# Kernel optimization log

Hardware: AMD Instinct MI355X
Metric: run time of the kernel (lower is better)

## Reference

```python
import jax, jax.numpy as jnp
import numpy as np
import math

B, N, D, H = 32, 512, 512, 8
DK = D // H
MAX_DIST = 100.0
BINS = 20
BIN_SIZE = MAX_DIST / BINS


def setup_inputs() -> dict:
    key = jax.random.key(0)
    ks = jax.random.split(key, 12)
    s = 1.0 / math.sqrt(D)
    inp = {
        "x": jax.random.normal(ks[0], (B, N, D), dtype=jnp.float32),
        "distance_matrix": jax.random.uniform(ks[1], (B, N, N), dtype=jnp.float32) * MAX_DIST,
        "Wq": jax.random.uniform(ks[2], (D, D), jnp.float32, -s, s),
        "bq": jax.random.uniform(ks[3], (D,), jnp.float32, -s, s),
        "Wk": jax.random.uniform(ks[4], (D, D), jnp.float32, -s, s),
        "bk": jax.random.uniform(ks[5], (D,), jnp.float32, -s, s),
        "Wv": jax.random.uniform(ks[6], (D, D), jnp.float32, -s, s),
        "bv": jax.random.uniform(ks[7], (D,), jnp.float32, -s, s),
        "Wo": jax.random.uniform(ks[8], (D, D), jnp.float32, -s, s),
        "bo": jax.random.uniform(ks[9], (D,), jnp.float32, -s, s),
        "dist_weights": jnp.ones((BINS + 1,), dtype=jnp.float32),
    }
    return inp


def reference(x, distance_matrix, Wq, bq, Wk, bk, Wv, bv, Wo, bo, dist_weights):
    temperature = 1.0
    # Linear projections; torch nn.Linear computes x @ W.T + b
    q = (x @ Wq.T + bq).reshape(B, N, H, DK).transpose(0, 2, 1, 3)  # [B,H,N,DK]
    k = (x @ Wk.T + bk).reshape(B, N, H, DK).transpose(0, 2, 1, 3)
    v = (x @ Wv.T + bv).reshape(B, N, H, DK).transpose(0, 2, 1, 3)

    scores = jnp.einsum("bhqd,bhkd->bhqk", q, k) / math.sqrt(DK)  # [B,H,N,N]

    # Relative position bias: bin distances, look up scalar weight per pair
    binned = jnp.clip((distance_matrix / BIN_SIZE).astype(jnp.int32), 0, BINS)  # [B,N,N]
    bias = dist_weights[binned] / temperature  # [B,N,N]
    scores = scores + bias[:, None, :, :]  # broadcast over heads

    attn = jax.nn.softmax(scores, axis=-1)  # dropout is identity in eval
    out = jnp.einsum("bhqk,bhkd->bhqd", attn, v)  # [B,H,N,DK]
    out = out.transpose(0, 2, 1, 3).reshape(B, N, D)
    return out @ Wo.T + bo
```

## Files before the change

kernel.cpp:

```cpp
#include <hip/hip_runtime.h>
#include <hip/hip_fp16.h>
#include <math.h>
#include <stdint.h>

#define BB 32
#define NN 512
#define DDIM 512
#define HH 8
#define DK 64

typedef __attribute__((ext_vector_type(8))) short short8;
typedef __attribute__((ext_vector_type(8))) _Float16 half8;
typedef __attribute__((ext_vector_type(2))) _Float16 half2v;
typedef __attribute__((ext_vector_type(4))) float floatx4;
typedef unsigned short ushort_t;
typedef unsigned int uint_t;

__device__ __forceinline__ void gl_lds16(const void* g, void* l) {
    __builtin_amdgcn_global_load_lds(
        (const __attribute__((address_space(1))) uint_t*)g,
        (__attribute__((address_space(3))) uint_t*)l,
        16, 0, 0);
}

__device__ __forceinline__ ushort_t f2bf(float f) {
    uint_t u = __builtin_bit_cast(uint_t, f);
    u += 0x7fff + ((u >> 16) & 1);
    return (ushort_t)(u >> 16);
}

__device__ __forceinline__ uint_t pkbf(float a, float b) {
    return (uint_t)f2bf(a) | ((uint_t)f2bf(b) << 16);
}

__device__ __forceinline__ uint_t pkh(float a, float b) {
    return __builtin_bit_cast(uint_t, __builtin_amdgcn_cvt_pkrtz(a, b));
}

__device__ __forceinline__ float h2f(ushort_t u) {
    return __half2float(__ushort_as_half(u));
}

__global__ __launch_bounds__(256) void cvt_bf16(const float* __restrict__ s,
                                                ushort_t* __restrict__ d, int n8) {
    const int i = blockIdx.x * 256 + threadIdx.x;
    if (i >= n8) return;
    const float4 a = ((const float4*)s)[i * 2 + 0];
    const float4 b = ((const float4*)s)[i * 2 + 1];
    uint4 o;
    o.x = pkbf(a.x, a.y); o.y = pkbf(a.z, a.w);
    o.z = pkbf(b.x, b.y); o.w = pkbf(b.z, b.w);
    *(uint4*)(d + i * 8) = o;
}

__global__ __launch_bounds__(256) void cvt_w4(
    const float* __restrict__ w0, const float* __restrict__ w1,
    const float* __restrict__ w2, const float* __restrict__ w3,
    ushort_t* __restrict__ o0, ushort_t* __restrict__ o1,
    ushort_t* __restrict__ o2, ushort_t* __restrict__ o3) {
    const float* s; ushort_t* d;
    if (blockIdx.y == 0)      { s = w0; d = o0; }
    else if (blockIdx.y == 1) { s = w1; d = o1; }
    else if (blockIdx.y == 2) { s = w2; d = o2; }
    else                      { s = w3; d = o3; }
    const int i = blockIdx.x * 256 + threadIdx.x;
    const float4 a = ((const float4*)s)[i * 2 + 0];
    const float4 b = ((const float4*)s)[i * 2 + 1];
    uint4 o;
    o.x = pkbf(a.x, a.y); o.y = pkbf(a.z, a.w);
    o.z = pkbf(b.x, b.y); o.w = pkbf(b.z, b.w);
    *(uint4*)(d + i * 8) = o;
}

__global__ __launch_bounds__(256) void bias_half(const float* __restrict__ dist,
                                                 const float* __restrict__ dw,
                                                 ushort_t* __restrict__ T, int n8) {
    __shared__ float dws[21];
    if (threadIdx.x < 21) dws[threadIdx.x] = (dw[threadIdx.x] - 3.0f) * 1.44269504f;
    __syncthreads();
    const int i = blockIdx.x * 256 + threadIdx.x;
    if (i >= n8) return;
    float dv[8];
    { const float4 a = ((const float4*)dist)[i * 2 + 0];
      const float4 b = ((const float4*)dist)[i * 2 + 1];
      dv[0]=a.x; dv[1]=a.y; dv[2]=a.z; dv[3]=a.w;
      dv[4]=b.x; dv[5]=b.y; dv[6]=b.z; dv[7]=b.w; }
    ushort_t h[8];
    #pragma unroll
    for (int j = 0; j < 8; ++j) {
        int bin = (int)(dv[j] / 5.0f);
        bin = bin < 0 ? 0 : (bin > 20 ? 20 : bin);
        h[j] = __half_as_ushort(__float2half(dws[bin]));
    }
    uint4 o;
    o.x = (uint_t)h[0] | ((uint_t)h[1] << 16);
    o.y = (uint_t)h[2] | ((uint_t)h[3] << 16);
    o.z = (uint_t)h[4] | ((uint_t)h[5] << 16);
    o.w = (uint_t)h[6] | ((uint_t)h[7] << 16);
    *(uint4*)(T + i * 8) = o;
}

__global__ __launch_bounds__(256) void transp_v(const ushort_t* __restrict__ V,
                                                ushort_t* __restrict__ Vt) {
    __shared__ ushort_t T[64][72];
    const int tid = threadIdx.x;
    const int q0 = blockIdx.x * 64;
    const int bh = blockIdx.y, b = bh >> 3, h = bh & 7;
    #pragma unroll
    for (int rnd = 0; rnd < 2; ++rnd) {
        const int idx = rnd * 256 + tid;
        const int row = idx >> 3, c8 = (idx & 7) * 8;
        const uint4 v = *(const uint4*)&V[((size_t)(b * NN + q0 + row)) * DDIM + h * DK + c8];
        ushort_t* t = &T[row][c8];
        t[0] = (ushort_t)v.x; t[1] = (ushort_t)(v.x >> 16);
        t[2] = (ushort_t)v.y; t[3] = (ushort_t)(v.y >> 16);
        t[4] = (ushort_t)v.z; t[5] = (ushort_t)(v.z >> 16);
        t[6] = (ushort_t)v.w; t[7] = (ushort_t)(v.w >> 16);
    }
    __syncthreads();
    #pragma unroll
    for (int rnd = 0; rnd < 2; ++rnd) {
        const int idx = rnd * 256 + tid;
        const int d = idx >> 3, q8 = (idx & 7) * 8;
        uint4 o;
        o.x = (uint_t)T[q8 + 0][d] | ((uint_t)T[q8 + 1][d] << 16);
        o.y = (uint_t)T[q8 + 2][d] | ((uint_t)T[q8 + 3][d] << 16);
        o.z = (uint_t)T[q8 + 4][d] | ((uint_t)T[q8 + 5][d] << 16);
        o.w = (uint_t)T[q8 + 6][d] | ((uint_t)T[q8 + 7][d] << 16);
        *(uint4*)&Vt[((size_t)(bh * DK + d)) * NN + q0 + q8] = o;
    }
}

#define GEMM_CORE(Aptr, Wptr)                                                           \
    __shared__ ushort_t As[128 * 32];                                                   \
    __shared__ ushort_t Bs[128 * 32];                                                   \
    const int tid = threadIdx.x;                                                        \
    const int lane = tid & 63, wid = tid >> 6;                                          \
    const int quad = lane >> 4, l15 = lane & 15;                                        \
    const int m0 = blockIdx.x * 128, n0 = blockIdx.y * 128;                             \
    const int wy = wid >> 1, wx = wid & 1;                                              \
    floatx4 acc[4][4];                                                                  \
    _Pragma("unroll") for (int i = 0; i < 4; ++i)                                       \
        _Pragma("unroll") for (int j = 0; j < 4; ++j)                                   \
            _Pragma("unroll") for (int r = 0; r < 4; ++r) acc[i][j][r] = 0.f;           \
    for (int k0 = 0; k0 < DDIM; k0 += 32) {                                             \
        __syncthreads();                                                                \
        _Pragma("unroll") for (int j = 0; j < 4; ++j) {                                 \
            const int t = wid * 4 + j;                                                  \
            const int rowi = ((t & 7) << 4) + (lane >> 2);                              \
            const int cd = (lane & 3) ^ ((rowi >> 1) & 3);                              \
            if (t < 8)                                                                  \
                gl_lds16(Aptr + (size_t)(m0 + rowi) * DDIM + k0 + cd * 8,               \
                         (char*)As + ((t & 7) << 10));                                  \
            else                                                                        \
                gl_lds16(Wptr + (size_t)(n0 + rowi) * DDIM + k0 + cd * 8,               \
                         (char*)Bs + ((t & 7) << 10));                                  \
        }                                                                               \
        __syncthreads();                                                                \
        short8 aw[4], bt[4];                                                            \
        _Pragma("unroll") for (int fi = 0; fi < 4; ++fi) {                              \
            const int r = wy * 64 + fi * 16 + l15;                                      \
            aw[fi] = *(const short8*)((const char*)Bs + r * 64 +                        \
                                      ((quad ^ ((r >> 1) & 3)) << 4));                  \
        }                                                                               \
        _Pragma("unroll") for (int ti = 0; ti < 4; ++ti) {                              \
            const int r = wx * 64 + ti * 16 + l15;                                      \
            bt[ti] = *(const short8*)((const char*)As + r * 64 +                        \
                                      ((quad ^ ((r >> 1) & 3)) << 4));                  \
        }                                                                               \
        _Pragma("unroll") for (int fi = 0; fi < 4; ++fi)                                \
            _Pragma("unroll") for (int ti = 0; ti < 4; ++ti)                            \
                acc[fi][ti] = __builtin_amdgcn_mfma_f32_16x16x32_bf16(                  \
                    aw[fi], bt[ti], acc[fi][ti], 0, 0, 0);                              \
    }

__global__ __launch_bounds__(256) void gemm_qkv(
    const ushort_t* __restrict__ A,
    const ushort_t* __restrict__ W0, const ushort_t* __restrict__ W1,
    const ushort_t* __restrict__ W2,
    const float* __restrict__ b0, const float* __restrict__ b1,
    const float* __restrict__ b2,
    ushort_t* __restrict__ o0, ushort_t* __restrict__ o1, ushort_t* __restrict__ o2) {
    const ushort_t* W; const float* bias; ushort_t* dst;
    if (blockIdx.z == 0)      { W = W0; bias = b0; dst = o0; }
    else if (blockIdx.z == 1) { W = W1; bias = b1; dst = o1; }
    else                      { W = W2; bias = b2; dst = o2; }
    const bool as_f16 = (blockIdx.z == 2);
    GEMM_CORE(A, W)
    #pragma unroll
    for (int fi = 0; fi < 4; ++fi) {
        const int f = n0 + wy * 64 + fi * 16 + quad * 4;
        const float4 b4 = *(const float4*)&bias[f];
        #pragma unroll
        for (int ti = 0; ti < 4; ++ti) {
            const int token = m0 + wx * 64 + ti * 16 + l15;
            const float v0 = acc[fi][ti][0] + b4.x, v1 = acc[fi][ti][1] + b4.y;
            const float v2 = acc[fi][ti][2] + b4.z, v3 = acc[fi][ti][3] + b4.w;
            uint2 v;
            if (as_f16) { v.x = pkh(v0, v1);  v.y = pkh(v2, v3); }
            else        { v.x = pkbf(v0, v1); v.y = pkbf(v2, v3); }
            *(uint2*)&dst[(size_t)token * DDIM + f] = v;
        }
    }
}

__global__ __launch_bounds__(256) void gemm_out(
    const ushort_t* __restrict__ A, const ushort_t* __restrict__ Wo,
    const float* __restrict__ bo, float* __restrict__ dst) {
    GEMM_CORE(A, Wo)
    #pragma unroll
    for (int fi = 0; fi < 4; ++fi) {
        const int f = n0 + wy * 64 + fi * 16 + quad * 4;
        const float4 b4 = *(const float4*)&bo[f];
        #pragma unroll
        for (int ti = 0; ti < 4; ++ti) {
            const int token = m0 + wx * 64 + ti * 16 + l15;
            float4 v;
            v.x = acc[fi][ti][0] + b4.x; v.y = acc[fi][ti][1] + b4.y;
            v.z = acc[fi][ti][2] + b4.z; v.w = acc[fi][ti][3] + b4.w;
            *(float4*)&dst[(size_t)token * DDIM + f] = v;
        }
    }
}

__global__ __launch_bounds__(512, 2) void attn_fused(
    const ushort_t* __restrict__ Qg, const ushort_t* __restrict__ Kg,
    const ushort_t* __restrict__ Vtg, const ushort_t* __restrict__ Tg,
    ushort_t* __restrict__ aout) {
    __shared__ ushort_t Ks[512 * 64];
    __shared__ ushort_t Vs[64 * 512];
    __shared__ ushort_t Ps[8 * 1024];

    const int tid = threadIdx.x, lane = tid & 63, wid = tid >> 6;
    const int quad = lane >> 4, l15 = lane & 15;
    const int h = blockIdx.x, b = blockIdx.y;
    const float K1 = 0.18033688f;

    #pragma unroll
    for (int j = 0; j < 8; ++j) {
        const int t = wid * 8 + j;
        {
            const int row = t * 8 + (lane >> 3);
            const int key = (row & 7) ^ ((row >> 3) & 7);
            const int g = (lane & 7) ^ key;
            gl_lds16(Kg + (size_t)(b * NN + row) * DDIM + h * DK + g * 8,
                     (char*)Ks + t * 1024);
        }
        {
            const int key = (t & 7) ^ ((t >> 3) & 7);
            const int g = lane ^ key;
            gl_lds16(Vtg + (size_t)((b * HH + h) * DK + t) * NN + g * 8,
                     (char*)Vs + t * 1024);
        }
    }

    short8 bq[4][2];
    #pragma unroll
    for (int qs = 0; qs < 4; ++qs) {
        const ushort_t* qp =
            Qg + (size_t)(b * NN + wid * 64 + qs * 16 + l15) * DDIM + h * DK;
        bq[qs][0] = *(const short8*)(qp + quad * 8);
        bq[qs][1] = *(const short8*)(qp + 32 + quad * 8);
    }

    float lsum[4] = {0.f, 0.f, 0.f, 0.f};
    floatx4 O[4][4];
    #pragma unroll
    for (int qs = 0; qs < 4; ++qs)
        #pragma unroll
        for (int ni = 0; ni < 4; ++ni)
            #pragma unroll
            for (int r = 0; r < 4; ++r) O[qs][ni][r] = 0.f;

    char* const pbase = (char*)Ps + wid * 2048;
    const int swk = l15 & 7;

    __syncthreads();

    for (int kt = 0; kt < 8; ++kt) {
        uint2 tv[4][4];
        #pragma unroll
        for (int qs = 0; qs < 4; ++qs) {
            const ushort_t* tp =
                Tg + (size_t)(b * NN + wid * 64 + qs * 16 + l15) * NN + kt * 64;
            #pragma unroll
            for (int f = 0; f < 4; ++f)
                tv[qs][f] = *(const uint2*)(tp + f * 16 + quad * 4);
        }
        short8 kf[2][4];
        #pragma unroll
        for (int ks = 0; ks < 2; ++ks)
            #pragma unroll
            for (int f = 0; f < 4; ++f) {
                const int row = kt * 64 + f * 16 + l15;
                const int key = (row & 7) ^ ((row >> 3) & 7);
                kf[ks][f] = *(const short8*)((const char*)Ks + row * 128 +
                                             (((ks * 4 + quad) ^ key) << 4));
            }
        half8 vf[2][4];
        #pragma unroll
        for (int ks = 0; ks < 2; ++ks)
            #pragma unroll
            for (int ni = 0; ni < 4; ++ni) {
                const int d = ni * 16 + l15;
                const int key = (d & 7) ^ ((d >> 3) & 7);
                const int c = (kt * 8 + ks * 4 + quad) ^ key;
                vf[ks][ni] = *(const half8*)((const char*)Vs + d * 1024 + (c << 4));
            }

        #pragma unroll
        for (int qs = 0; qs < 4; ++qs) {
            floatx4 S[4];
            #pragma unroll
            for (int f = 0; f < 4; ++f)
                #pragma unroll
                for (int r = 0; r < 4; ++r) S[f][r] = 0.f;
            #pragma unroll
            for (int ks = 0; ks < 2; ++ks)
                #pragma unroll
                for (int f = 0; f < 4; ++f)
                    S[f] = __builtin_amdgcn_mfma_f32_16x16x32_bf16(
                        kf[ks][f], bq[qs][ks], S[f], 0, 0, 0);

            float ls = 0.f;
            #pragma unroll
            for (int f = 0; f < 4; ++f) {
                const float t0 = h2f((ushort_t)(tv[qs][f].x));
                const float t1 = h2f((ushort_t)(tv[qs][f].x >> 16));
                const float t2 = h2f((ushort_t)(tv[qs][f].y));
                const float t3 = h2f((ushort_t)(tv[qs][f].y >> 16));
                const float p0 = exp2f(S[f][0] * K1 + t0);
                const float p1 = exp2f(S[f][1] * K1 + t1);
                const float p2 = exp2f(S[f][2] * K1 + t2);
                const float p3 = exp2f(S[f][3] * K1 + t3);
                ls += (p0 + p1) + (p2 + p3);
                uint2 pw;
                pw.x = pkh(p0, p1);
                pw.y = pkh(p2, p3);
                *(uint2*)(pbase + l15 * 128 +
                          (((f * 4 + quad) ^ (swk << 1)) << 3)) = pw;
            }
            lsum[qs] += ls;

            #pragma unroll
            for (int ks = 0; ks < 2; ++ks) {
                const half8 bp = *(const half8*)(pbase + l15 * 128 +
                                                 (((ks * 4 + quad) ^ swk) << 4));
                #pragma unroll
                for (int ni = 0; ni < 4; ++ni)
                    O[qs][ni] = __builtin_amdgcn_mfma_f32_16x16x32_f16(
                        vf[ks][ni], bp, O[qs][ni], 0, 0, 0);
            }
        }
    }

    #pragma unroll
    for (int qs = 0; qs < 4; ++qs) {
        float l = lsum[qs];
        l += __shfl_xor(l, 16);
        l += __shfl_xor(l, 32);
        const float inv = 1.0f / l;
        const size_t orow =
            (size_t)(b * NN + wid * 64 + qs * 16 + l15) * DDIM + h * DK;
        #pragma unroll
        for (int ni = 0; ni < 4; ++ni) {
            uint2 ov;
            ov.x = pkbf(O[qs][ni][0] * inv, O[qs][ni][1] * inv);
            ov.y = pkbf(O[qs][ni][2] * inv, O[qs][ni][3] * inv);
            *(uint2*)&aout[orow + ni * 16 + quad * 4] = ov;
        }
    }
}

extern "C" void kernel_launch(void* const* d_in, const int* in_sizes, int n_in,
                              void* d_out, int out_size, void* d_ws, size_t ws_size,
                              hipStream_t stream) {
    const float* x    = (const float*)d_in[0];
    const float* dist = (const float*)d_in[1];
    const float* Wq   = (const float*)d_in[2];
    const float* bq   = (const float*)d_in[3];
    const float* Wk   = (const float*)d_in[4];
    const float* bk   = (const float*)d_in[5];
    const float* Wv   = (const float*)d_in[6];
    const float* bv   = (const float*)d_in[7];
    const float* Wo   = (const float*)d_in[8];
    const float* bo   = (const float*)d_in[9];
    const float* dw   = (const float*)d_in[10];
    float* out = (float*)d_out;

    const size_t NELT = (size_t)BB * NN * DDIM;
    ushort_t* xb  = (ushort_t*)d_ws;
    ushort_t* wqb = xb + NELT;
    ushort_t* wkb = wqb + DDIM * DDIM;
    ushort_t* wvb = wkb + DDIM * DDIM;
    ushort_t* wob = wvb + DDIM * DDIM;
    ushort_t* qb  = wob + DDIM * DDIM;
    ushort_t* kb  = qb + NELT;
    ushort_t* vb  = kb + NELT;
    ushort_t* vt  = vb + NELT;
    ushort_t* Tm  = vt + NELT;
    ushort_t* ab  = xb;

    cvt_bf16<<<4096, 256, 0, stream>>>(x, xb, (int)(NELT / 8));
    cvt_w4<<<dim3(128, 4), 256, 0, stream>>>(Wq, Wk, Wv, Wo, wqb, wkb, wvb, wob);
    bias_half<<<4096, 256, 0, stream>>>(dist, dw, Tm, (int)(NELT / 8));

    gemm_qkv<<<dim3(128, 4, 3), 256, 0, stream>>>(xb, wqb, wkb, wvb, bq, bk, bv,
                                                  qb, kb, vb);
    transp_v<<<dim3(8, 256), 256, 0, stream>>>(vb, vt);
    attn_fused<<<dim3(HH, BB), 512, 0, stream>>>(qb, kb, vt, Tm, ab);
    gemm_out<<<dim3(128, 4), 256, 0, stream>>>(ab, wob, bo, out);
}
```

Baseline: 245.9 us.

## Switch attention to 32x32 MFMA tiles with in-register P via permlane swap

Rewrites the fused attention inner loop to use 32x32x16 MFMA instructions in place of 16x16x32, reorganizing Q, K, V and bias fragment layouts to match. The P matrix is no longer round-tripped through shared memory: packed fp16 probabilities are exchanged between half-waves with permlane32_swap to form the B operand directly. It also adds s_setprio around the MFMA groups. This removes LDS writes and reads plus their latency for P and halves the number of MFMA issues, at the cost of larger accumulator register tiles that may pressure occupancy.

```diff
diff --git a/kernel.cpp b/kernel.cpp
--- a/kernel.cpp
+++ b/kernel.cpp
@@ -13,6 +13,7 @@
 typedef __attribute__((ext_vector_type(8))) _Float16 half8;
 typedef __attribute__((ext_vector_type(2))) _Float16 half2v;
 typedef __attribute__((ext_vector_type(4))) float floatx4;
+typedef __attribute__((ext_vector_type(16))) float floatx16;
 typedef unsigned short ushort_t;
 typedef unsigned int uint_t;
 
@@ -229,10 +230,9 @@
     ushort_t* __restrict__ aout) {
     __shared__ ushort_t Ks[512 * 64];
     __shared__ ushort_t Vs[64 * 512];
-    __shared__ ushort_t Ps[8 * 1024];
 
     const int tid = threadIdx.x, lane = tid & 63, wid = tid >> 6;
-    const int quad = lane >> 4, l15 = lane & 15;
+    const int l31 = lane & 31, hl = lane >> 5;
     const int h = blockIdx.x, b = blockIdx.y;
     const float K1 = 0.18033688f;
 
@@ -254,121 +254,137 @@
         }
     }
 
-    short8 bq[4][2];
-    #pragma unroll
-    for (int qs = 0; qs < 4; ++qs) {
+    short8 bq[2][4];
+    #pragma unroll
+    for (int qt = 0; qt < 2; ++qt) {
         const ushort_t* qp =
-            Qg + (size_t)(b * NN + wid * 64 + qs * 16 + l15) * DDIM + h * DK;
-        bq[qs][0] = *(const short8*)(qp + quad * 8);
-        bq[qs][1] = *(const short8*)(qp + 32 + quad * 8);
-    }
-
-    float lsum[4] = {0.f, 0.f, 0.f, 0.f};
-    floatx4 O[4][4];
-    #pragma unroll
-    for (int qs = 0; qs < 4; ++qs)
-        #pragma unroll
-        for (int ni = 0; ni < 4; ++ni)
-            #pragma unroll
-            for (int r = 0; r < 4; ++r) O[qs][ni][r] = 0.f;
-
-    char* const pbase = (char*)Ps + wid * 2048;
-    const int swk = l15 & 7;
+            Qg + (size_t)(b * NN + wid * 64 + qt * 32 + l31) * DDIM + h * DK + hl * 8;
+        #pragma unroll
+        for (int st = 0; st < 4; ++st) bq[qt][st] = *(const short8*)(qp + st * 16);
+    }
+
+    float lsum[2] = {0.f, 0.f};
+    floatx16 O[2][2];
+    #pragma unroll
+    for (int qt = 0; qt < 2; ++qt)
+        #pragma unroll
+        for (int dt = 0; dt < 2; ++dt)
+            #pragma unroll
+            for (int r = 0; r < 16; ++r) O[qt][dt][r] = 0.f;
 
     __syncthreads();
 
     for (int kt = 0; kt < 8; ++kt) {
-        uint2 tv[4][4];
-        #pragma unroll
-        for (int qs = 0; qs < 4; ++qs) {
+        uint2 tv[2][2][4];
+        #pragma unroll
+        for (int qt = 0; qt < 2; ++qt) {
             const ushort_t* tp =
-                Tg + (size_t)(b * NN + wid * 64 + qs * 16 + l15) * NN + kt * 64;
-            #pragma unroll
-            for (int f = 0; f < 4; ++f)
-                tv[qs][f] = *(const uint2*)(tp + f * 16 + quad * 4);
-        }
+                Tg + (size_t)(b * NN + wid * 64 + qt * 32 + l31) * NN + kt * 64 + hl * 4;
+            #pragma unroll
+            for (int kti = 0; kti < 2; ++kti)
+                #pragma unroll
+                for (int g = 0; g < 4; ++g)
+                    tv[qt][kti][g] = *(const uint2*)(tp + kti * 32 + g * 8);
+        }
+
         short8 kf[2][4];
         #pragma unroll
-        for (int ks = 0; ks < 2; ++ks)
-            #pragma unroll
-            for (int f = 0; f < 4; ++f) {
-                const int row = kt * 64 + f * 16 + l15;
-                const int key = (row & 7) ^ ((row >> 3) & 7);
-                kf[ks][f] = *(const short8*)((const char*)Ks + row * 128 +
-                                             (((ks * 4 + quad) ^ key) << 4));
+        for (int kti = 0; kti < 2; ++kti) {
+            const int row = kt * 64 + kti * 32 + l31;
+            const int key = (row & 7) ^ ((row >> 3) & 7);
+            #pragma unroll
+            for (int st = 0; st < 4; ++st)
+                kf[kti][st] = *(const short8*)((const char*)Ks + row * 128 +
+                                               (((st * 2 + hl) ^ key) << 4));
+        }
+
+        half8 vf[2][2][2];
+        #pragma unroll
+        for (int dt = 0; dt < 2; ++dt) {
+            const int d = dt * 32 + l31;
+            const int key = (d & 7) ^ ((d >> 3) & 7);
+            #pragma unroll
+            for (int kti = 0; kti < 2; ++kti)
+                #pragma unroll
+                for (int ks = 0; ks < 2; ++ks)
+                    vf[kti][dt][ks] = *(const half8*)((const char*)Vs + d * 1024 +
+                        (((kt * 8 + kti * 4 + ks * 2 + hl) ^ key) << 4));
+        }
+
+        #pragma unroll
+        for (int qt = 0; qt < 2; ++qt)
+            #pragma unroll
+            for (int kti = 0; kti < 2; ++kti) {
+                floatx16 S;
+                #pragma unroll
+                for (int r = 0; r < 16; ++r) S[r] = 0.f;
+                __builtin_amdgcn_s_setprio(1);
+                #pragma unroll
+                for (int st = 0; st < 4; ++st)
+                    S = __builtin_amdgcn_mfma_f32_32x32x16_bf16(
+                        kf[kti][st], bq[qt][st], S, 0, 0, 0);
+                __builtin_amdgcn_s_setprio(0);
+
+                float ls = 0.f;
+                #pragma unroll
+                for (int ks = 0; ks < 2; ++ks) {
+                    float pp[8];
+                    #pragma unroll
+                    for (int gg = 0; gg < 2; ++gg) {
+                        const uint2 tg = tv[qt][kti][ks * 2 + gg];
+                        const float t0 = h2f((ushort_t)tg.x);
+                        const float t1 = h2f((ushort_t)(tg.x >> 16));
+                        const float t2 = h2f((ushort_t)tg.y);
+                        const float t3 = h2f((ushort_t)(tg.y >> 16));
+                        const int sb = ks * 8 + gg * 4;
+                        pp[gg * 4 + 0] = exp2f(S[sb + 0] * K1 + t0);
+                        pp[gg * 4 + 1] = exp2f(S[sb + 1] * K1 + t1);
+                        pp[gg * 4 + 2] = exp2f(S[sb + 2] * K1 + t2);
+                        pp[gg * 4 + 3] = exp2f(S[sb + 3] * K1 + t3);
+                        ls += (pp[gg * 4 + 0] + pp[gg * 4 + 1]) +
+                              (pp[gg * 4 + 2] + pp[gg * 4 + 3]);
+                    }
+                    uint_t w0 = pkh(pp[0], pp[1]);
+                    uint_t w1 = pkh(pp[2], pp[3]);
+                    uint_t w2 = pkh(pp[4], pp[5]);
+                    uint_t w3 = pkh(pp[6], pp[7]);
+                    auto r02 = __builtin_amdgcn_permlane32_swap(w0, w2, false, false);
+                    auto r13 = __builtin_amdgcn_permlane32_swap(w1, w3, false, false);
+                    uint4 uu;
+                    uu.x = r02[0];
+                    uu.y = r13[0];
+                    uu.z = r02[1];
+                    uu.w = r13[1];
+                    const half8 bp = __builtin_bit_cast(half8, uu);
+
+                    __builtin_amdgcn_s_setprio(1);
+                    #pragma unroll
+                    for (int dt = 0; dt < 2; ++dt)
+                        O[qt][dt] = __builtin_amdgcn_mfma_f32_32x32x16_f16(
+                            vf[kti][dt][ks], bp, O[qt][dt], 0, 0, 0);
+                    __builtin_amdgcn_s_setprio(0);
+                }
+                lsum[qt] += ls;
             }
-        half8 vf[2][4];
-        #pragma unroll
-        for (int ks = 0; ks < 2; ++ks)
-            #pragma unroll
-            for (int ni = 0; ni < 4; ++ni) {
-                const int d = ni * 16 + l15;
-                const int key = (d & 7) ^ ((d >> 3) & 7);
-                const int c = (kt * 8 + ks * 4 + quad) ^ key;
-                vf[ks][ni] = *(const half8*)((const char*)Vs + d * 1024 + (c << 4));
-            }
-
-        #pragma unroll
-        for (int qs = 0; qs < 4; ++qs) {
-            floatx4 S[4];
-            #pragma unroll
-            for (int f = 0; f < 4; ++f)
-                #pragma unroll
-                for (int r = 0; r < 4; ++r) S[f][r] = 0.f;
-            #pragma unroll
-            for (int ks = 0; ks < 2; ++ks)
-                #pragma unroll
-                for (int f = 0; f < 4; ++f)
-                    S[f] = __builtin_amdgcn_mfma_f32_16x16x32_bf16(
-                        kf[ks][f], bq[qs][ks], S[f], 0, 0, 0);
-
-            float ls = 0.f;
-            #pragma unroll
-            for (int f = 0; f < 4; ++f) {
-                const float t0 = h2f((ushort_t)(tv[qs][f].x));
-                const float t1 = h2f((ushort_t)(tv[qs][f].x >> 16));
-                const float t2 = h2f((ushort_t)(tv[qs][f].y));
-                const float t3 = h2f((ushort_t)(tv[qs][f].y >> 16));
-                const float p0 = exp2f(S[f][0] * K1 + t0);
-                const float p1 = exp2f(S[f][1] * K1 + t1);
-                const float p2 = exp2f(S[f][2] * K1 + t2);
-                const float p3 = exp2f(S[f][3] * K1 + t3);
-                ls += (p0 + p1) + (p2 + p3);
-                uint2 pw;
-                pw.x = pkh(p0, p1);
-                pw.y = pkh(p2, p3);
-                *(uint2*)(pbase + l15 * 128 +
-                          (((f * 4 + quad) ^ (swk << 1)) << 3)) = pw;
-            }
-            lsum[qs] += ls;
-
-            #pragma unroll
-            for (int ks = 0; ks < 2; ++ks) {
-                const half8 bp = *(const half8*)(pbase + l15 * 128 +
-                                                 (((ks * 4 + quad) ^ swk) << 4));
-                #pragma unroll
-                for (int ni = 0; ni < 4; ++ni)
-                    O[qs][ni] = __builtin_amdgcn_mfma_f32_16x16x32_f16(
-                        vf[ks][ni], bp, O[qs][ni], 0, 0, 0);
-            }
-        }
-    }
-
-    #pragma unroll
-    for (int qs = 0; qs < 4; ++qs) {
-        float l = lsum[qs];
-        l += __shfl_xor(l, 16);
+    }
+
+    #pragma unroll
+    for (int qt = 0; qt < 2; ++qt) {
+        float l = lsum[qt];
         l += __shfl_xor(l, 32);
         const float inv = 1.0f / l;
         const size_t orow =
-            (size_t)(b * NN + wid * 64 + qs * 16 + l15) * DDIM + h * DK;
-        #pragma unroll
-        for (int ni = 0; ni < 4; ++ni) {
-            uint2 ov;
-            ov.x = pkbf(O[qs][ni][0] * inv, O[qs][ni][1] * inv);
-            ov.y = pkbf(O[qs][ni][2] * inv, O[qs][ni][3] * inv);
-            *(uint2*)&aout[orow + ni * 16 + quad * 4] = ov;
-        }
+            (size_t)(b * NN + wid * 64 + qt * 32 + l31) * DDIM + h * DK;
+        #pragma unroll
+        for (int dt = 0; dt < 2; ++dt)
+            #pragma unroll
+            for (int g = 0; g < 4; ++g) {
+                const int d = dt * 32 + g * 8 + hl * 4;
+                uint2 ov;
+                ov.x = pkbf(O[qt][dt][g * 4 + 0] * inv, O[qt][dt][g * 4 + 1] * inv);
+                ov.y = pkbf(O[qt][dt][g * 4 + 2] * inv, O[qt][dt][g * 4 + 3] * inv);
+                *(uint2*)&aout[orow + d] = ov;
+            }
     }
 }
 
```

Result: slower. 271.2 us (+10.3%).
